# Kernel optimization log

Measured on AMD Instinct MI355X. Metric: run time of the kernel, lower is better.

## Reference

```python
import jax, jax.numpy as jnp
import numpy as np

D_MODEL = 256
NHEAD = 8
HEAD_DIM = D_MODEL // NHEAD
EPS_ATTN = 1e-6
EPS_LN = 1e-5


def _layernorm(x, g, b):
    mu = jnp.mean(x, axis=-1, keepdims=True)
    var = jnp.mean(jnp.square(x - mu), axis=-1, keepdims=True)
    return (x - mu) * jax.lax.rsqrt(var + EPS_LN) * g + b


def _embed_rotary(t, cos, sin):
    # t, cos, sin: [N, L, C]; interleaved pair rotation as in RoFPE.embed_rotary
    t2 = jnp.stack([-t[..., 1::2], t[..., ::2]], axis=-1).reshape(t.shape)
    return t * cos + t2 * sin


def setup_inputs() -> dict:
    key = jax.random.key(0)
    ks = jax.random.split(key, 12)
    N, L, S, C = 4, 4800, 4800, D_MODEL
    w = lambda k, shp: jax.random.normal(k, shp, dtype=jnp.float32) * 0.05
    return {
        "x": jax.random.normal(ks[0], (N, L, C), dtype=jnp.float32),
        "source": jax.random.normal(ks[1], (N, S, C), dtype=jnp.float32),
        "x_pe": jax.random.normal(ks[2], (N, L, C, 2), dtype=jnp.float32),
        "source_pe": jax.random.normal(ks[3], (N, S, C, 2), dtype=jnp.float32),
        "Wq": w(ks[4], (C, C)),
        "Wk": w(ks[5], (C, C)),
        "Wv": w(ks[6], (C, C)),
        "Wm": w(ks[7], (C, C)),
        "W1": w(ks[8], (2 * C, 2 * C)),
        "W2": w(ks[9], (C, 2 * C)),
        "g1": jnp.ones((C,), dtype=jnp.float32),
        "b1": jnp.zeros((C,), dtype=jnp.float32),
        "g2": jnp.ones((C,), dtype=jnp.float32),
        "b2": jnp.zeros((C,), dtype=jnp.float32),
    }


def reference(x, source, x_pe, source_pe, Wq, Wk, Wv, Wm, W1, W2, g1, b1, g2, b2):
    bs, L, C = x.shape
    H, D = NHEAD, HEAD_DIM
    # projections (nn.Linear: y = x @ W.T)
    q = x @ Wq.T
    k = source @ Wk.T
    v = source @ Wv.T
    # inline rotary PE
    q = _embed_rotary(q, x_pe[..., 0], x_pe[..., 1]).reshape(bs, L, H, D)
    k = _embed_rotary(k, source_pe[..., 0], source_pe[..., 1]).reshape(bs, -1, H, D)
    v = v.reshape(bs, -1, H, D)
    # LoFTR linear attention: phi(x) = elu(x) + 1
    Q = jax.nn.elu(q) + 1.0
    K = jax.nn.elu(k) + 1.0
    v_len = v.shape[1]
    vals = v / v_len
    KV = jnp.einsum("nshd,nshv->nhdv", K, vals)          # [N,H,D,D]
    Z = 1.0 / (jnp.einsum("nlhd,nhd->nlh", Q, K.sum(axis=1)) + EPS_ATTN)
    msg = jnp.einsum("nlhd,nhdv,nlh->nlhv", Q, KV, Z) * v_len  # [N,L,H,D]
    # merge + norm1
    msg = msg.reshape(bs, L, H * D) @ Wm.T
    msg = _layernorm(msg, g1, b1)
    # concat-MLP + norm2 + residual
    h = jnp.concatenate([x, msg], axis=-1)               # [N,L,2C]
    h = jax.nn.relu(h @ W1.T) @ W2.T
    h = _layernorm(h, g2, b2)
    return x + h
```

## Files before the change

### kernel.cpp

```cpp
#include <hip/hip_runtime.h>
#include <hip/hip_bf16.h>
#include <math.h>

#define NROWS 19200
#define SLEN  4800
#define KV_CHUNKS 50
#define KV_SC     96

typedef unsigned short ushort_t;
typedef __attribute__((ext_vector_type(8))) short bf16x8;
typedef __attribute__((ext_vector_type(4))) float f32x4;
typedef __attribute__((ext_vector_type(8))) unsigned short ushort8;

__device__ __forceinline__ float bf2f(ushort_t u) {
  union { unsigned int i; float f; } x; x.i = ((unsigned int)u) << 16; return x.f;
}
__device__ __forceinline__ ushort_t f2bf(float f) {
  __hip_bfloat16 h = __float2bfloat16(f);
  union { __hip_bfloat16 h; ushort_t u; } x; x.h = h; return x.u;
}

#define GLOAD16(g, l) __builtin_amdgcn_global_load_lds( \
    (const __attribute__((address_space(1))) unsigned int*)(g), \
    (__attribute__((address_space(3))) unsigned int*)(l), 16, 0, 0)

template <int EPI, bool CONCAT>
__device__ __forceinline__ void gemmT_body(
    const ushort_t* __restrict__ A0, const ushort_t* __restrict__ A1,
    const ushort_t* __restrict__ W, ushort_t* __restrict__ outp,
    int Nn, int K, int bm, int bn, char* smem) {
  const int tid = threadIdx.x;
  const int wave = tid >> 6, lane = tid & 63;
  const int wm = (wave >> 1) * 64, wn = (wave & 1) * 64;
  const int l15 = lane & 15, l4 = lane >> 4;

  f32x4 acc[4][4];
#pragma unroll
  for (int i = 0; i < 4; ++i)
#pragma unroll
    for (int j = 0; j < 4; ++j) acc[i][j] = (f32x4){0.f, 0.f, 0.f, 0.f};

  for (int k0 = 0; k0 < K; k0 += 64) {
    const ushort_t* Asrc;
    int ka;
    if (CONCAT) { Asrc = (k0 < 256) ? A0 : A1; ka = k0 & 255; }
    else        { Asrc = A0; ka = k0; }
#pragma unroll
    for (int c = 0; c < 4; ++c) {
      int ch = c * 4 + wave;
      int o = ch * 1024 + lane * 16;
      int row = o >> 7, g = (o >> 4) & 7;
      const ushort_t* sp =
          Asrc + (size_t)(bm + row) * 256 + ka + ((g ^ (row & 7)) << 3);
      GLOAD16(sp, smem + ch * 1024);
    }
#pragma unroll
    for (int c = 0; c < 4; ++c) {
      int ch = c * 4 + wave;
      int o = ch * 1024 + lane * 16;
      int row = o >> 7, g = (o >> 4) & 7;
      const ushort_t* sp =
          W + (size_t)(bn + row) * K + k0 + ((g ^ (row & 7)) << 3);
      GLOAD16(sp, smem + 16384 + ch * 1024);
    }
    __syncthreads();
#pragma unroll
    for (int kc = 0; kc < 2; ++kc) {
      bf16x8 af[4], bfr[4];
#pragma unroll
      for (int mi = 0; mi < 4; ++mi) {
        int r = wm + mi * 16 + l15;
        int G = kc * 4 + l4;
        af[mi] = *(const bf16x8*)(smem + r * 128 + ((G ^ (r & 7)) << 4));
      }
#pragma unroll
      for (int ni = 0; ni < 4; ++ni) {
        int r = wn + ni * 16 + l15;
        int G = kc * 4 + l4;
        bfr[ni] = *(const bf16x8*)(smem + 16384 + r * 128 +
                                   ((G ^ (r & 7)) << 4));
      }
#pragma unroll
      for (int mi = 0; mi < 4; ++mi)
#pragma unroll
        for (int ni = 0; ni < 4; ++ni)
          acc[mi][ni] = __builtin_amdgcn_mfma_f32_16x16x32_bf16(
              af[mi], bfr[ni], acc[mi][ni], 0, 0, 0);
    }
    __syncthreads();
  }

  ushort_t* st = (ushort_t*)smem;
#pragma unroll
  for (int mi = 0; mi < 4; ++mi)
#pragma unroll
    for (int ni = 0; ni < 4; ++ni)
#pragma unroll
      for (int j = 0; j < 4; ++j) {
        int trow = wm + mi * 16 + l4 * 4 + j;
        int tcol = wn + ni * 16 + l15;
        float v = acc[mi][ni][j];
        if (EPI == 3) v = fmaxf(v, 0.f);
        st[trow * 140 + tcol] = f2bf(v);
      }
  __syncthreads();
#pragma unroll
  for (int c = 0; c < 8; ++c) {
    int ch = c * 256 + tid;
    int row = ch >> 4, g = ch & 15;
    ushort8 u = *(const ushort8*)&st[row * 140 + g * 8];
    *(ushort8*)&outp[(size_t)(bm + row) * Nn + bn + g * 8] = u;
  }
}

__global__ __launch_bounds__(256) void qkv_fused(
    const ushort_t* __restrict__ xb, const ushort_t* __restrict__ srcb,
    const ushort_t* __restrict__ Wqb, const ushort_t* __restrict__ Wkb,
    const ushort_t* __restrict__ Wvb,
    ushort_t* __restrict__ Q, ushort_t* __restrict__ Kb,
    ushort_t* __restrict__ Vb) {
  extern __shared__ char smem[];
  int b = blockIdx.x;
  const int which = b < 300 ? 0 : (b < 600 ? 1 : 2);
  b -= which * 300;
  const int bm = (b >> 1) * 128, bn = (b & 1) * 128;
  const ushort_t* A = (which == 0) ? xb : srcb;
  const ushort_t* W = (which == 0) ? Wqb : (which == 1 ? Wkb : Wvb);
  ushort_t* o = (which == 0) ? Q : (which == 1 ? Kb : Vb);
  gemmT_body<0, false>(A, nullptr, W, o, 256, 256, bm, bn, smem);
}

__global__ __launch_bounds__(256) void mlp1_kernel(
    const ushort_t* __restrict__ xb, const ushort_t* __restrict__ msgln,
    const ushort_t* __restrict__ W1b, ushort_t* __restrict__ h1) {
  extern __shared__ char smem[];
  const int bm = (blockIdx.x >> 2) * 128, bn = (blockIdx.x & 3) * 128;
  gemmT_body<3, true>(xb, msgln, W1b, h1, 512, 512, bm, bn, smem);
}

__global__ __launch_bounds__(256) void msg_merge_ln(
    const ushort_t* __restrict__ Qb, const float* __restrict__ x_pe,
    const float* __restrict__ KV, const float* __restrict__ Ksum,
    const ushort_t* __restrict__ Wm,
    const float* __restrict__ g, const float* __restrict__ bb,
    ushort_t* __restrict__ msgln) {
  __shared__ char mem[33024];
  __shared__ char Bs[256 * 128];
  __shared__ float Ks[8][32];
  __shared__ float partS[4][32];
  __shared__ float partQ[4][32];
  __shared__ float gS[256], bS[256];

  const int tid = threadIdx.x;
  const int wave = tid >> 6, lane = tid & 63;
  const int l15 = lane & 15, l4 = lane >> 4;
  const int bm = blockIdx.x * 32;
  const int n = bm / SLEN;

  gS[tid] = g[tid];
  bS[tid] = bb[tid];
  Ks[tid >> 5][tid & 31] = Ksum[(n * 8 + (tid >> 5)) * 32 + (tid & 31)];

  float* phiQ = (float*)mem;
#pragma unroll
  for (int p = 0; p < 4; ++p) {
    int rr = p * 8 + (tid >> 5), cc = (tid & 31) * 8;
    const size_t eoff = (size_t)(bm + rr) * 256 + cc;
    const ushort8 uq = *(const ushort8*)&Qb[eoff];
    const float4* pp = (const float4*)&x_pe[eoff * 2];
    float4 p0 = pp[0], p1 = pp[1], p2 = pp[2], p3 = pp[3];
    float v[8];
#pragma unroll
    for (int i = 0; i < 8; ++i) v[i] = bf2f((ushort_t)uq[i]);
    float r[8];
    r[0] = v[0] * p0.x - v[1] * p0.y; r[1] = v[1] * p0.z + v[0] * p0.w;
    r[2] = v[2] * p1.x - v[3] * p1.y; r[3] = v[3] * p1.z + v[2] * p1.w;
    r[4] = v[4] * p2.x - v[5] * p2.y; r[5] = v[5] * p2.z + v[4] * p2.w;
    r[6] = v[6] * p3.x - v[7] * p3.y; r[7] = v[7] * p3.z + v[6] * p3.w;
#pragma unroll
    for (int i = 0; i < 8; ++i)
      v[i] = r[i] > 0.f ? r[i] + 1.f : __expf(r[i]);
    float* dst = &phiQ[rr * 258 + cc];
#pragma unroll
    for (int i = 0; i < 4; ++i)
      *(float2*)(dst + 2 * i) = (float2){v[2 * i], v[2 * i + 1]};
  }
  __syncthreads();

  const int h = tid >> 5, v = tid & 31;
  const float* kvh = &KV[(size_t)(n * 8 + h) * 1024 + v];
  float kvc[32];
#pragma unroll
  for (int d = 0; d < 32; ++d) kvc[d] = kvh[d * 32];
  ushort_t msge[32];
#pragma unroll
  for (int rr = 0; rr < 32; ++rr) {
    float z = 0.f, m = 0.f;
#pragma unroll
    for (int d = 0; d < 32; ++d) {
      float qd = phiQ[rr * 258 + h * 32 + d];
      z += qd * Ks[h][d];
      m += qd * kvc[d];
    }
    z = 1.0f / (z + 1e-6f);
    msge[rr] = f2bf(m * z);
  }
  __syncthreads();

  ushort_t* As = (ushort_t*)mem;
  const int col = tid;
  const int gi0 = col >> 3, cb = col & 7;
#pragma unroll
  for (int rr = 0; rr < 32; ++rr) {
    int gis = (gi0 & ~7) | ((gi0 & 7) ^ (rr & 7));
    As[rr * 256 + gis * 8 + cb] = msge[rr];
  }
  __syncthreads();

  f32x4 acc[2][4];
#pragma unroll
  for (int i = 0; i < 2; ++i)
#pragma unroll
    for (int j = 0; j < 4; ++j) acc[i][j] = (f32x4){0.f, 0.f, 0.f, 0.f};

  for (int k0 = 0; k0 < 256; k0 += 64) {
#pragma unroll
    for (int c = 0; c < 8; ++c) {
      int ch = c * 256 + tid;
      int row = ch >> 3, gch = ch & 7;
      const ushort_t* src =
          Wm + (size_t)row * 256 + k0 + ((gch ^ (row & 7)) << 3);
      GLOAD16(src, Bs + ch * 16);
    }
    __syncthreads();
#pragma unroll
    for (int kc = 0; kc < 2; ++kc) {
      bf16x8 af[2], bfr[4];
#pragma unroll
      for (int mi = 0; mi < 2; ++mi) {
        int r = mi * 16 + l15;
        int gi = (k0 >> 3) + kc * 4 + l4;
        int gis = (gi & ~7) | ((gi & 7) ^ (r & 7));
        af[mi] = *(const bf16x8*)(As + r * 256 + gis * 8);
      }
#pragma unroll
      for (int ni = 0; ni < 4; ++ni) {
        int r = wave * 64 + ni * 16 + l15;
        int G = kc * 4 + l4;
        bfr[ni] = *(const bf16x8*)(Bs + r * 128 + ((G ^ (r & 7)) << 4));
      }
#pragma unroll
      for (int mi = 0; mi < 2; ++mi)
#pragma unroll
        for (int ni = 0; ni < 4; ++ni)
          acc[mi][ni] = __builtin_amdgcn_mfma_f32_16x16x32_bf16(
              af[mi], bfr[ni], acc[mi][ni], 0, 0, 0);
    }
    __syncthreads();
  }

#pragma unroll
  for (int mi = 0; mi < 2; ++mi)
#pragma unroll
    for (int j = 0; j < 4; ++j) {
      float s = acc[mi][0][j] + acc[mi][1][j] + acc[mi][2][j] + acc[mi][3][j];
      float q = acc[mi][0][j] * acc[mi][0][j] + acc[mi][1][j] * acc[mi][1][j] +
                acc[mi][2][j] * acc[mi][2][j] + acc[mi][3][j] * acc[mi][3][j];
#pragma unroll
      for (int m = 1; m < 16; m <<= 1) {
        s += __shfl_xor(s, m);
        q += __shfl_xor(q, m);
      }
      if (l15 == 0) {
        int row = mi * 16 + l4 * 4 + j;
        partS[wave][row] = s;
        partQ[wave][row] = q;
      }
    }
  __syncthreads();

  float mu[2][4], rsv[2][4];
#pragma unroll
  for (int mi = 0; mi < 2; ++mi)
#pragma unroll
    for (int j = 0; j < 4; ++j) {
      int row = mi * 16 + l4 * 4 + j;
      float s = partS[0][row] + partS[1][row] + partS[2][row] + partS[3][row];
      float q2 = partQ[0][row] + partQ[1][row] + partQ[2][row] + partQ[3][row];
      float m_ = s * (1.f / 256.f);
      float var = q2 * (1.f / 256.f) - m_ * m_;
      mu[mi][j] = m_;
      rsv[mi][j] = rsqrtf(var + 1e-5f);
    }

#pragma unroll
  for (int mi = 0; mi < 2; ++mi)
#pragma unroll
    for (int ni = 0; ni < 4; ++ni)
#pragma unroll
      for (int j = 0; j < 4; ++j) {
        int row = mi * 16 + l4 * 4 + j;
        int col2 = wave * 64 + ni * 16 + l15;
        float vv = (acc[mi][ni][j] - mu[mi][j]) * rsv[mi][j] * gS[col2] +
                   bS[col2];
        msgln[(size_t)(bm + row) * 256 + col2] = f2bf(vv);
      }
}

template <int KDIM, bool RESID, bool OUTBF>
__global__ __launch_bounds__(256) void gemm_ln_kernel(
    const ushort_t* __restrict__ A, const ushort_t* __restrict__ W,
    const float* __restrict__ g, const float* __restrict__ bb,
    const float* __restrict__ resid, void* __restrict__ outp) {
  __shared__ char As[32 * 128];
  __shared__ char Bs[256 * 128];
  __shared__ float partS[4][32];
  __shared__ float partQ[4][32];
  __shared__ float gS[256], bS[256];

  const int tid = threadIdx.x;
  const int wave = tid >> 6, lane = tid & 63;
  const int l15 = lane & 15, l4 = lane >> 4;
  const int bm = blockIdx.x * 32;

  gS[tid] = g[tid];
  bS[tid] = bb[tid];

  f32x4 acc[2][4];
#pragma unroll
  for (int i = 0; i < 2; ++i)
#pragma unroll
    for (int j = 0; j < 4; ++j) acc[i][j] = (f32x4){0.f, 0.f, 0.f, 0.f};

  for (int k0 = 0; k0 < KDIM; k0 += 64) {
    {
      int row = tid >> 3, gch = tid & 7;
      const ushort_t* src =
          A + (size_t)(bm + row) * KDIM + k0 + ((gch ^ (row & 7)) << 3);
      GLOAD16(src, As + tid * 16);
    }
#pragma unroll
    for (int c = 0; c < 8; ++c) {
      int ch = c * 256 + tid;
      int row = ch >> 3, gch = ch & 7;
      const ushort_t* src =
          W + (size_t)row * KDIM + k0 + ((gch ^ (row & 7)) << 3);
      GLOAD16(src, Bs + ch * 16);
    }
    __syncthreads();
#pragma unroll
    for (int kc = 0; kc < 2; ++kc) {
      bf16x8 af[2], bfr[4];
#pragma unroll
      for (int mi = 0; mi < 2; ++mi) {
        int r = mi * 16 + l15;
        int G = kc * 4 + l4;
        af[mi] = *(const bf16x8*)(As + r * 128 + ((G ^ (r & 7)) << 4));
      }
#pragma unroll
      for (int ni = 0; ni < 4; ++ni) {
        int r = wave * 64 + ni * 16 + l15;
        int G = kc * 4 + l4;
        bfr[ni] = *(const bf16x8*)(Bs + r * 128 + ((G ^ (r & 7)) << 4));
      }
#pragma unroll
      for (int mi = 0; mi < 2; ++mi)
#pragma unroll
        for (int ni = 0; ni < 4; ++ni)
          acc[mi][ni] = __builtin_amdgcn_mfma_f32_16x16x32_bf16(
              af[mi], bfr[ni], acc[mi][ni], 0, 0, 0);
    }
    __syncthreads();
  }

#pragma unroll
  for (int mi = 0; mi < 2; ++mi)
#pragma unroll
    for (int j = 0; j < 4; ++j) {
      float s = acc[mi][0][j] + acc[mi][1][j] + acc[mi][2][j] + acc[mi][3][j];
      float q = acc[mi][0][j] * acc[mi][0][j] + acc[mi][1][j] * acc[mi][1][j] +
                acc[mi][2][j] * acc[mi][2][j] + acc[mi][3][j] * acc[mi][3][j];
#pragma unroll
      for (int m = 1; m < 16; m <<= 1) {
        s += __shfl_xor(s, m);
        q += __shfl_xor(q, m);
      }
      if (l15 == 0) {
        int row = mi * 16 + l4 * 4 + j;
        partS[wave][row] = s;
        partQ[wave][row] = q;
      }
    }
  __syncthreads();

  float mu[2][4], rsv[2][4];
#pragma unroll
  for (int mi = 0; mi < 2; ++mi)
#pragma unroll
    for (int j = 0; j < 4; ++j) {
      int row = mi * 16 + l4 * 4 + j;
      float s = partS[0][row] + partS[1][row] + partS[2][row] + partS[3][row];
      float q2 = partQ[0][row] + partQ[1][row] + partQ[2][row] + partQ[3][row];
      float m_ = s * (1.f / 256.f);
      float var = q2 * (1.f / 256.f) - m_ * m_;
      mu[mi][j] = m_;
      rsv[mi][j] = rsqrtf(var + 1e-5f);
    }

#pragma unroll
  for (int mi = 0; mi < 2; ++mi)
#pragma unroll
    for (int ni = 0; ni < 4; ++ni)
#pragma unroll
      for (int j = 0; j < 4; ++j) {
        int row = mi * 16 + l4 * 4 + j;
        int col = wave * 64 + ni * 16 + l15;
        float v = (acc[mi][ni][j] - mu[mi][j]) * rsv[mi][j] * gS[col] + bS[col];
        size_t gr = (size_t)(bm + row);
        if (RESID) v += resid[gr * 256 + col];
        if (OUTBF)
          ((ushort_t*)outp)[gr * 256 + col] = f2bf(v);
        else
          ((float*)outp)[gr * 256 + col] = v;
      }
}

__global__ __launch_bounds__(256) void kv_partial(
    const ushort_t* __restrict__ Kb, const ushort_t* __restrict__ Vb,
    const float* __restrict__ s_pe,
    float* __restrict__ kvp, float* __restrict__ ksp) {
  __shared__ float bufK[32][32];
  __shared__ float bufV[32][32];
  const int b = blockIdx.x;
  const int ch = b % KV_CHUNKS;
  const int nh = b / KV_CHUNKS;
  const int h = nh & 7, n = nh >> 3;
  const int tid = threadIdx.x;
  const int d = tid >> 3, vb = (tid & 7) * 4;
  const int half = tid >> 7, t = tid & 127;
  const int srow = t >> 2, seg = (t & 3) * 8;
  const int segS = (seg + 8 * (srow & 3)) & 31;
  float a0 = 0.f, a1 = 0.f, a2 = 0.f, a3 = 0.f, ks = 0.f;
  const size_t base = (size_t)n * SLEN * 256 + (size_t)h * 32;
  const int s0 = ch * KV_SC;
  for (int s = s0; s < s0 + KV_SC; s += 32) {
    __syncthreads();
    const size_t eoff = base + (size_t)(s + srow) * 256 + seg;
    ushort8 u = *(const ushort8*)((half ? Vb : Kb) + eoff);
    float v[8];
#pragma unroll
    for (int i = 0; i < 8; ++i) v[i] = bf2f((ushort_t)u[i]);
    if (!half) {
      const float4* pp = (const float4*)&s_pe[eoff * 2];
      float4 p0 = pp[0], p1 = pp[1], p2 = pp[2], p3 = pp[3];
      float r[8];
      r[0] = v[0] * p0.x - v[1] * p0.y; r[1] = v[1] * p0.z + v[0] * p0.w;
      r[2] = v[2] * p1.x - v[3] * p1.y; r[3] = v[3] * p1.z + v[2] * p1.w;
      r[4] = v[4] * p2.x - v[5] * p2.y; r[5] = v[5] * p2.z + v[4] * p2.w;
      r[6] = v[6] * p3.x - v[7] * p3.y; r[7] = v[7] * p3.z + v[6] * p3.w;
#pragma unroll
      for (int i = 0; i < 8; ++i)
        v[i] = r[i] > 0.f ? r[i] + 1.f : __expf(r[i]);
    }
    float* dst = half ? &bufV[srow][segS] : &bufK[srow][segS];
    *(float4*)dst = (float4){v[0], v[1], v[2], v[3]};
    *(float4*)(dst + 4) = (float4){v[4], v[5], v[6], v[7]};
    __syncthreads();
#pragma unroll
    for (int ss = 0; ss < 32; ++ss) {
      int rot = 8 * (ss & 3);
      float kd = bufK[ss][(d + rot) & 31];
      float4 vv = *(const float4*)&bufV[ss][(vb + rot) & 31];
      a0 += kd * vv.x; a1 += kd * vv.y; a2 += kd * vv.z; a3 += kd * vv.w;
      ks += kd;
    }
  }
  float* kv = &kvp[(size_t)b * 1024 + d * 32 + vb];
  kv[0] = a0; kv[1] = a1; kv[2] = a2; kv[3] = a3;
  if ((tid & 7) == 0) ksp[(size_t)b * 32 + d] = ks;
}

__global__ __launch_bounds__(256) void kv_reduce(
    const float* __restrict__ kvp, const float* __restrict__ ksp,
    float* __restrict__ KV, float* __restrict__ Ksum) {
  const int nh = blockIdx.x;
  const int tid = threadIdx.x;
  for (int e = tid; e < 1024; e += 256) {
    float s = 0.f;
    for (int p = 0; p < KV_CHUNKS; ++p)
      s += kvp[(size_t)(nh * KV_CHUNKS + p) * 1024 + e];
    KV[(size_t)nh * 1024 + e] = s;
  }
  if (tid < 32) {
    float s = 0.f;
    for (int p = 0; p < KV_CHUNKS; ++p)
      s += ksp[(size_t)(nh * KV_CHUNKS + p) * 32 + tid];
    Ksum[nh * 32 + tid] = s;
  }
}

__global__ __launch_bounds__(256) void conv_all(
    const float* __restrict__ x, const float* __restrict__ src,
    const float* w0, const float* w1, const float* w2, const float* w3,
    const float* w4, const float* w5,
    ushort_t* __restrict__ xo, ushort_t* __restrict__ so,
    ushort_t* o0, ushort_t* o1, ushort_t* o2, ushort_t* o3, ushort_t* o4,
    ushort_t* o5) {
  int blk = blockIdx.x;
  if (blk < 4800) {
    const float* s; ushort_t* d;
    if (blk < 2400) { s = x; d = xo; } else { s = src; d = so; blk -= 2400; }
    size_t o = ((size_t)blk * 256 + threadIdx.x) * 8;
    float4 v0 = *(const float4*)&s[o];
    float4 v1 = *(const float4*)&s[o + 4];
    ushort8 u = {f2bf(v0.x), f2bf(v0.y), f2bf(v0.z), f2bf(v0.w),
                 f2bf(v1.x), f2bf(v1.y), f2bf(v1.z), f2bf(v1.w)};
    *(ushort8*)&d[o] = u;
  } else {
    int e = ((blk - 4800) * 256 + threadIdx.x) * 4;
    const float* s; ushort_t* d; int off;
    if      (e < 65536)  { s = w0; d = o0; off = e; }
    else if (e < 131072) { s = w1; d = o1; off = e - 65536; }
    else if (e < 196608) { s = w2; d = o2; off = e - 131072; }
    else if (e < 262144) { s = w3; d = o3; off = e - 196608; }
    else if (e < 524288) { s = w4; d = o4; off = e - 262144; }
    else                 { s = w5; d = o5; off = e - 524288; }
    float4 v = *(const float4*)&s[off];
    ushort4 u = make_ushort4(f2bf(v.x), f2bf(v.y), f2bf(v.z), f2bf(v.w));
    *(ushort4*)&d[off] = u;
  }
}

extern "C" void kernel_launch(void* const* d_in, const int* in_sizes, int n_in,
                              void* d_out, int out_size, void* d_ws,
                              size_t ws_size, hipStream_t stream) {
  const float* x    = (const float*)d_in[0];
  const float* src  = (const float*)d_in[1];
  const float* x_pe = (const float*)d_in[2];
  const float* s_pe = (const float*)d_in[3];
  const float* Wq = (const float*)d_in[4];
  const float* Wk = (const float*)d_in[5];
  const float* Wv = (const float*)d_in[6];
  const float* Wm = (const float*)d_in[7];
  const float* W1 = (const float*)d_in[8];
  const float* W2 = (const float*)d_in[9];
  const float* g1 = (const float*)d_in[10];
  const float* b1 = (const float*)d_in[11];
  const float* g2 = (const float*)d_in[12];
  const float* b2 = (const float*)d_in[13];
  float* out = (float*)d_out;

  const size_t R = (size_t)NROWS * 256;
  ushort_t* xb    = (ushort_t*)d_ws;
  ushort_t* srcb  = xb + R;
  ushort_t* Qb    = srcb + R;
  ushort_t* Kb    = Qb + R;
  ushort_t* Vb    = Kb + R;
  ushort_t* msgln = Vb + R;
  ushort_t* Wqb   = msgln + R;
  ushort_t* Wkb   = Wqb + 65536;
  ushort_t* Wvb   = Wkb + 65536;
  ushort_t* Wmb   = Wvb + 65536;
  ushort_t* W1b   = Wmb + 65536;
  ushort_t* W2b   = W1b + 262144;
  float* kvp      = (float*)(W2b + 131072);
  float* ksp      = kvp + 1638400;
  float* KVb      = ksp + 51200;
  float* Ksum     = KVb + 32768;
  ushort_t* h1   = Kb;

  dim3 blk(256);
  conv_all<<<5440, blk, 0, stream>>>(x, src, Wq, Wk, Wv, Wm, W1, W2,
                                     xb, srcb, Wqb, Wkb, Wvb, Wmb, W1b, W2b);
  qkv_fused<<<900, blk, 35840, stream>>>(xb, srcb, Wqb, Wkb, Wvb, Qb, Kb, Vb);
  kv_partial<<<1600, blk, 0, stream>>>(Kb, Vb, s_pe, kvp, ksp);
  kv_reduce<<<32, blk, 0, stream>>>(kvp, ksp, KVb, Ksum);
  msg_merge_ln<<<600, blk, 0, stream>>>(Qb, x_pe, KVb, Ksum, Wmb, g1, b1,
                                        msgln);
  mlp1_kernel<<<600, blk, 35840, stream>>>(xb, msgln, W1b, h1);
  gemm_ln_kernel<512, true, false><<<600, blk, 0, stream>>>(
      h1, W2b, g2, b2, x, out);
}
```

Before: 132.9 us.

## Compute attention message with MFMA using bf16 phiQ and KV in LDS

The msg_merge_ln kernel now stores phi(Q) as swizzled bf16 in LDS and converts the per-batch KV matrices to bf16 in shared memory. The per-head Q·KV product then runs on MFMA instructions instead of scalar FMA loops, and the normalizer Z is computed separately per row and head. The Wm GEMM stage is re-tiled to k-steps of 32 so the larger shared-memory footprint still fits. This removes the heavy scalar inner loop and register pressure, at the cost of bf16 rounding of phi(Q) and KV and extra sync stages.

```diff
diff --git a/kernel.cpp b/kernel.cpp
--- a/kernel.cpp
+++ b/kernel.cpp
@@ -144,9 +144,11 @@
     const ushort_t* __restrict__ Wm,
     const float* __restrict__ g, const float* __restrict__ bb,
     ushort_t* __restrict__ msgln) {
-  __shared__ char mem[33024];
-  __shared__ char Bs[256 * 128];
+  __shared__ ushort_t AsM[32 * 256];
+  __shared__ ushort_t KVb[8 * 1024];
+  __shared__ ushort_t Bs[256 * 32];
   __shared__ float Ks[8][32];
+  __shared__ float zS[32][8];
   __shared__ float partS[4][32];
   __shared__ float partQ[4][32];
   __shared__ float gS[256], bS[256];
@@ -161,7 +163,15 @@
   bS[tid] = bb[tid];
   Ks[tid >> 5][tid & 31] = Ksum[(n * 8 + (tid >> 5)) * 32 + (tid & 31)];
 
-  float* phiQ = (float*)mem;
+#pragma unroll
+  for (int c = 0; c < 8; ++c) {
+    int e4 = c * 256 + tid;
+    const float4 kv4 = *(const float4*)&KV[(size_t)(n * 8) * 1024 + e4 * 4];
+    ushort4 u = make_ushort4(f2bf(kv4.x), f2bf(kv4.y), f2bf(kv4.z),
+                             f2bf(kv4.w));
+    *(ushort4*)&KVb[e4 * 4] = u;
+  }
+
 #pragma unroll
   for (int p = 0; p < 4; ++p) {
     int rr = p * 8 + (tid >> 5), cc = (tid & 31) * 8;
@@ -177,85 +187,116 @@
     r[2] = v[2] * p1.x - v[3] * p1.y; r[3] = v[3] * p1.z + v[2] * p1.w;
     r[4] = v[4] * p2.x - v[5] * p2.y; r[5] = v[5] * p2.z + v[4] * p2.w;
     r[6] = v[6] * p3.x - v[7] * p3.y; r[7] = v[7] * p3.z + v[6] * p3.w;
-#pragma unroll
-    for (int i = 0; i < 8; ++i)
-      v[i] = r[i] > 0.f ? r[i] + 1.f : __expf(r[i]);
-    float* dst = &phiQ[rr * 258 + cc];
-#pragma unroll
-    for (int i = 0; i < 4; ++i)
-      *(float2*)(dst + 2 * i) = (float2){v[2 * i], v[2 * i + 1]};
+    ushort8 pk;
+#pragma unroll
+    for (int i = 0; i < 8; ++i) {
+      float w = r[i] > 0.f ? r[i] + 1.f : __expf(r[i]);
+      pk[i] = f2bf(w);
+    }
+    int gi = cc >> 3;
+    int gis = (gi & ~7) | ((gi & 7) ^ (rr & 7));
+    *(ushort8*)&AsM[rr * 256 + gis * 8] = pk;
   }
   __syncthreads();
 
-  const int h = tid >> 5, v = tid & 31;
-  const float* kvh = &KV[(size_t)(n * 8 + h) * 1024 + v];
-  float kvc[32];
-#pragma unroll
-  for (int d = 0; d < 32; ++d) kvc[d] = kvh[d * 32];
-  ushort_t msge[32];
-#pragma unroll
-  for (int rr = 0; rr < 32; ++rr) {
-    float z = 0.f, m = 0.f;
+  {
+    int row = tid >> 3, h = tid & 7;
+    float z = 0.f;
 #pragma unroll
     for (int d = 0; d < 32; ++d) {
-      float qd = phiQ[rr * 258 + h * 32 + d];
-      z += qd * Ks[h][d];
-      m += qd * kvc[d];
-    }
-    z = 1.0f / (z + 1e-6f);
-    msge[rr] = f2bf(m * z);
+      int gi = h * 4 + (d >> 3);
+      int gis = (gi & ~7) | ((gi & 7) ^ (row & 7));
+      z += bf2f(AsM[row * 256 + gis * 8 + (d & 7)]) * Ks[h][d];
+    }
+    zS[row][h] = 1.0f / (z + 1e-6f);
   }
   __syncthreads();
 
-  ushort_t* As = (ushort_t*)mem;
-  const int col = tid;
-  const int gi0 = col >> 3, cb = col & 7;
-#pragma unroll
-  for (int rr = 0; rr < 32; ++rr) {
-    int gis = (gi0 & ~7) | ((gi0 & 7) ^ (rr & 7));
-    As[rr * 256 + gis * 8 + cb] = msge[rr];
+  f32x4 macc[2][2][2];
+#pragma unroll
+  for (int hh2 = 0; hh2 < 2; ++hh2) {
+    const int h = wave * 2 + hh2;
+    bf16x8 af[2], bfr[2];
+#pragma unroll
+    for (int mi = 0; mi < 2; ++mi) {
+      int r = mi * 16 + l15;
+      int gi = h * 4 + l4;
+      int gis = (gi & ~7) | ((gi & 7) ^ (r & 7));
+      af[mi] = *(const bf16x8*)&AsM[r * 256 + gis * 8];
+    }
+#pragma unroll
+    for (int ni = 0; ni < 2; ++ni) {
+      int v = ni * 16 + l15;
+      const ushort_t* kvb = &KVb[h * 1024 + v];
+      bf16x8 t;
+#pragma unroll
+      for (int i = 0; i < 8; ++i) t[i] = (short)kvb[(l4 * 8 + i) * 32];
+      bfr[ni] = t;
+    }
+#pragma unroll
+    for (int mi = 0; mi < 2; ++mi)
+#pragma unroll
+      for (int ni = 0; ni < 2; ++ni)
+        macc[hh2][mi][ni] = __builtin_amdgcn_mfma_f32_16x16x32_bf16(
+            af[mi], bfr[ni], (f32x4){0.f, 0.f, 0.f, 0.f}, 0, 0, 0);
   }
   __syncthreads();
 
+#pragma unroll
+  for (int hh2 = 0; hh2 < 2; ++hh2) {
+    const int h = wave * 2 + hh2;
+#pragma unroll
+    for (int mi = 0; mi < 2; ++mi)
+#pragma unroll
+      for (int ni = 0; ni < 2; ++ni)
+#pragma unroll
+        for (int j = 0; j < 4; ++j) {
+          int row = mi * 16 + l4 * 4 + j;
+          int col = h * 32 + ni * 16 + l15;
+          float mv = macc[hh2][mi][ni][j] * zS[row][h];
+          int gi = col >> 3;
+          int gis = (gi & ~7) | ((gi & 7) ^ (row & 7));
+          AsM[row * 256 + gis * 8 + (col & 7)] = f2bf(mv);
+        }
+  }
+  __syncthreads();
+
   f32x4 acc[2][4];
 #pragma unroll
   for (int i = 0; i < 2; ++i)
 #pragma unroll
     for (int j = 0; j < 4; ++j) acc[i][j] = (f32x4){0.f, 0.f, 0.f, 0.f};
 
-  for (int k0 = 0; k0 < 256; k0 += 64) {
-#pragma unroll
-    for (int c = 0; c < 8; ++c) {
+  for (int k0 = 0; k0 < 256; k0 += 32) {
+#pragma unroll
+    for (int c = 0; c < 4; ++c) {
       int ch = c * 256 + tid;
-      int row = ch >> 3, gch = ch & 7;
+      int row = ch >> 2, gch = ch & 3;
       const ushort_t* src =
-          Wm + (size_t)row * 256 + k0 + ((gch ^ (row & 7)) << 3);
-      GLOAD16(src, Bs + ch * 16);
-    }
-    __syncthreads();
-#pragma unroll
-    for (int kc = 0; kc < 2; ++kc) {
-      bf16x8 af[2], bfr[4];
-#pragma unroll
-      for (int mi = 0; mi < 2; ++mi) {
-        int r = mi * 16 + l15;
-        int gi = (k0 >> 3) + kc * 4 + l4;
-        int gis = (gi & ~7) | ((gi & 7) ^ (r & 7));
-        af[mi] = *(const bf16x8*)(As + r * 256 + gis * 8);
-      }
-#pragma unroll
-      for (int ni = 0; ni < 4; ++ni) {
-        int r = wave * 64 + ni * 16 + l15;
-        int G = kc * 4 + l4;
-        bfr[ni] = *(const bf16x8*)(Bs + r * 128 + ((G ^ (r & 7)) << 4));
-      }
-#pragma unroll
-      for (int mi = 0; mi < 2; ++mi)
-#pragma unroll
-        for (int ni = 0; ni < 4; ++ni)
-          acc[mi][ni] = __builtin_amdgcn_mfma_f32_16x16x32_bf16(
-              af[mi], bfr[ni], acc[mi][ni], 0, 0, 0);
-    }
+          Wm + (size_t)row * 256 + k0 + ((gch ^ (row & 3)) << 3);
+      GLOAD16(src, (char*)Bs + ch * 16);
+    }
+    __syncthreads();
+    bf16x8 af[2], bfr[4];
+#pragma unroll
+    for (int mi = 0; mi < 2; ++mi) {
+      int r = mi * 16 + l15;
+      int gi = (k0 >> 3) + l4;
+      int gis = (gi & ~7) | ((gi & 7) ^ (r & 7));
+      af[mi] = *(const bf16x8*)&AsM[r * 256 + gis * 8];
+    }
+#pragma unroll
+    for (int ni = 0; ni < 4; ++ni) {
+      int r = wave * 64 + ni * 16 + l15;
+      int gs = l4 ^ (r & 3);
+      bfr[ni] = *(const bf16x8*)&Bs[r * 32 + gs * 8];
+    }
+#pragma unroll
+    for (int mi = 0; mi < 2; ++mi)
+#pragma unroll
+      for (int ni = 0; ni < 4; ++ni)
+        acc[mi][ni] = __builtin_amdgcn_mfma_f32_16x16x32_bf16(
+            af[mi], bfr[ni], acc[mi][ni], 0, 0, 0);
     __syncthreads();
   }
 
```

Result: faster. 121.8 us (-8.3%).
